# Optimization experiments

Measured on AMD Instinct MI355X. Metric: run time of the kernel, lower is better.

## Reference

```python
import jax, jax.numpy as jnp
import numpy as np

# single species, e3tb basis 1s+1p+1d
FLIST = [1, 3, 5]           # flistnorbs (spin_factor = 1 pre-doubling)
NORB = 9                    # full_basis_norb
SPIN = 2                    # spin_deg -> block doubled
A, E, K = 192, 3072, 4
P = 58                      # sum_{i<=j} iorb*jorb = 1+3+5+9+15+25


def setup_inputs() -> dict:
    key = jax.random.key(0)
    ks = jax.random.split(key, 6)
    return dict(
        orbpair_hopping=jax.random.normal(ks[0], (E, P), jnp.float32),
        orbpair_onsite=jax.random.normal(ks[1], (A, P), jnp.float32),
        R_matrix=jax.random.normal(ks[2], (A, SPIN * NORB, SPIN * NORB), jnp.float32) * 0.1,
        kpoints=jax.random.uniform(ks[3], (K, 3), jnp.float32),
        edge_cell_shift=jax.random.normal(ks[4], (E, 3), jnp.float32),
        edge_index=jax.random.randint(ks[5], (2, E), 0, A, jnp.int64),
    )


def _assemble(feats):
    """Scatter flat orbpair features into upper-triangular [*, NORB, NORB] blocks."""
    n = feats.shape[0]
    H = jnp.zeros((n, NORB, NORB), feats.dtype)
    offs = np.concatenate([[0], np.cumsum(FLIST)])
    p = 0
    for i in range(len(FLIST)):
        for j in range(i, len(FLIST)):
            io, jo = FLIST[i], FLIST[j]
            f = 0.5 if i == j else 1.0  # diagonal orbpairs get 0.5 (hermitianized later)
            H = H.at[:, offs[i]:offs[i] + io, offs[j]:offs[j] + jo].set(
                f * feats[:, p:p + io * jo].reshape(n, io, jo))
            p += io * jo
    return H


def _spin_double(H):
    # H[:, :, 0, :, 0] = H[:, :, 1, :, 1] = H  (kron with eye(2), interleaved layout)
    n = H.shape[0]
    return jnp.einsum('aij,st->aisjt', H, jnp.eye(2, dtype=H.dtype)).reshape(n, SPIN * NORB, SPIN * NORB)


def reference(orbpair_hopping, orbpair_onsite, R_matrix, kpoints, edge_cell_shift, edge_index):
    s = SPIN * NORB
    src, dst = edge_index[0], edge_index[1]

    onsite = _spin_double(_assemble(orbpair_onsite))      # [A, s, s]
    hop = _spin_double(_assemble(orbpair_hopping))        # [E, s, s]

    # rotate: R @ H @ R^T (gathered per-edge for hoppings)
    onsite = jnp.einsum('aip,apq,ajq->aij', R_matrix, onsite, R_matrix)
    hop = jnp.einsum('eip,epq,ejq->eij', R_matrix[src], hop, R_matrix[dst])

    # Bloch phases exp(-2*pi*i k.S) per (k, edge)
    phase = jnp.exp(-2j * jnp.pi * (kpoints @ edge_cell_shift.T)).astype(jnp.complex64)  # [K, E]

    contrib = hop[None].astype(jnp.complex64) * phase[:, :, None, None]  # [K, E, s, s]
    pair = src * A + dst
    blk = jax.vmap(lambda c: jax.ops.segment_sum(c, pair, num_segments=A * A))(contrib)
    blk = blk.reshape(K, A, A, s, s)

    idx = jnp.arange(A)
    blk = blk.at[:, idx, idx].add(onsite[None].astype(jnp.complex64))  # onsite on diag, all k

    Hk = blk.transpose(0, 1, 3, 2, 4).reshape(K, A * s, A * s)
    return Hk + jnp.conj(jnp.swapaxes(Hk, 1, 2))
```

## Files before the change

kernel.cpp:

```cpp
#include <hip/hip_runtime.h>

#define PFEAT 58
#define S18   18
#define ENT   324
#define MAXE  128

__device__ __constant__ unsigned char c_row[PFEAT] = {
    0,0,0,0,0,0,0,0,0,
    1,1,1,2,2,2,3,3,3,
    1,1,1,1,1,2,2,2,2,2,3,3,3,3,3,
    4,4,4,4,4,5,5,5,5,5,6,6,6,6,6,7,7,7,7,7,8,8,8,8,8};
__device__ __constant__ unsigned char c_col[PFEAT] = {
    0,1,2,3,4,5,6,7,8,
    1,2,3,1,2,3,1,2,3,
    4,5,6,7,8,4,5,6,7,8,4,5,6,7,8,
    4,5,6,7,8,4,5,6,7,8,4,5,6,7,8,4,5,6,7,8,4,5,6,7,8};
__device__ __constant__ float c_fac[PFEAT] = {
    0.5f,1,1,1,1,1,1,1,1,
    0.5f,0.5f,0.5f,0.5f,0.5f,0.5f,0.5f,0.5f,0.5f,
    1,1,1,1,1,1,1,1,1,1,1,1,1,1,1,
    0.5f,0.5f,0.5f,0.5f,0.5f,0.5f,0.5f,0.5f,0.5f,0.5f,0.5f,0.5f,0.5f,
    0.5f,0.5f,0.5f,0.5f,0.5f,0.5f,0.5f,0.5f,0.5f,0.5f,0.5f,0.5f};

__device__ __forceinline__ bool detect_i64(const int* __restrict__ ei) {
    const uint2* p = (const uint2*)ei;
    unsigned acc = 0u;
#pragma unroll 8
    for (int m = 0; m < 64; ++m) acc |= p[m].y;
    return acc == 0u;
}

__device__ __forceinline__ int load_idx(const int* __restrict__ ei, int pos,
                                        bool is64, int A) {
    int v = is64 ? ei[2 * pos] : ei[pos];
    v = v < 0 ? 0 : (v >= A ? A - 1 : v);
    return v;
}

__device__ __forceinline__ void assemble_rotate(
    const float* __restrict__ feat, const float* __restrict__ Rs,
    const float* __restrict__ Rd, float* sH9, float* sRs, float* sRd,
    float* sT, float* sM, int t, int nthreads)
{
    for (int idx = t; idx < ENT; idx += nthreads) { sRs[idx] = Rs[idx]; sRd[idx] = Rd[idx]; }
    if (t < 81) sH9[t] = 0.f;
    __syncthreads();
    if (t < PFEAT) sH9[c_row[t] * 9 + c_col[t]] = c_fac[t] * feat[t];
    __syncthreads();

    for (int idx = t; idx < ENT; idx += nthreads) {
        const int pp = idx / S18, q = idx - pp * S18;
        const int i = pp >> 1, u = pp & 1;
        float acc = 0.f;
#pragma unroll
        for (int j = 0; j < 9; ++j)
            acc += sH9[i * 9 + j] * sRd[q * S18 + 2 * j + u];
        sT[idx] = acc;
    }
    __syncthreads();

    for (int idx = t; idx < ENT; idx += nthreads) {
        const int p = idx / S18, q = idx - p * S18;
        float acc = 0.f;
#pragma unroll
        for (int pp = 0; pp < S18; ++pp)
            acc += sRs[p * S18 + pp] * sT[pp * S18 + q];
        sM[idx] = acc;
    }
}


__global__ __launch_bounds__(256) void build_csr_kernel(
    const int* __restrict__ ei, int E, int A,
    int* __restrict__ offsets,
    int2* __restrict__ entries)
{
    extern __shared__ int smem[];
    int* scnt = smem;
    int* scur = smem + A;
    __shared__ int sflag;
    const int t = threadIdx.x;
    if (t == 0) sflag = detect_i64(ei) ? 1 : 0;
    for (int a = t; a < A; a += 256) scnt[a] = 0;
    __syncthreads();
    const bool s64 = sflag != 0;
    for (int e = t; e < E; e += 256) {
        const int a = load_idx(ei, e, s64, A);
        const int b = load_idx(ei, E + e, s64, A);
        atomicAdd(&scnt[a], 1);
        atomicAdd(&scnt[b], 1);
    }
    __syncthreads();
    if (t == 0) {
        int acc = 0;
        for (int a = 0; a < A; ++a) { scur[a] = acc; acc += scnt[a]; }
    }
    __syncthreads();
    for (int a = t; a < A; a += 256) offsets[a] = scur[a];
    if (t == 0) offsets[A] = scur[A - 1] + scnt[A - 1];
    __syncthreads();
    for (int e = t; e < E; e += 256) {
        const int a = load_idx(ei, e, s64, A);
        const int b = load_idx(ei, E + e, s64, A);
        const int p = atomicAdd(&scur[a], 1);
        entries[p] = make_int2(e, b);
        const int q = atomicAdd(&scur[b], 1);
        entries[q] = make_int2(e | (1 << 30), a);
    }
}

__global__ __launch_bounds__(128) void rotate_kernel(
    const float* __restrict__ hop_feat, const float* __restrict__ ons_feat,
    const float* __restrict__ R, const int* __restrict__ ei,
    const float* __restrict__ kpts, const float* __restrict__ shift,
    float* __restrict__ hop_rot, float* __restrict__ hop_rotT,
    float* __restrict__ ons_rot, float* __restrict__ pcos,
    float* __restrict__ psin, int E, int A, int K, int hasT)
{
    __shared__ float sH9[81];
    __shared__ float sRs[ENT];
    __shared__ float sRd[ENT];
    __shared__ float sT[ENT];
    __shared__ float sM[ENT];
    __shared__ int   sflag;

    const int item = blockIdx.x;
    const int t = threadIdx.x;
    if (t == 0) sflag = detect_i64(ei) ? 1 : 0;
    __syncthreads();
    const bool s64 = sflag != 0;

    const float* feat; const float* Rs; const float* Rd; float* outp;
    if (item < E) {
        const int a_s = load_idx(ei, item, s64, A);
        const int a_d = load_idx(ei, E + item, s64, A);
        feat = hop_feat + (size_t)item * PFEAT;
        Rs = R + (size_t)a_s * ENT;
        Rd = R + (size_t)a_d * ENT;
        outp = hop_rot + (size_t)item * ENT;
        for (int k = t; k < K; k += 128) {
            const float dot = kpts[k * 3 + 0] * shift[3 * item + 0]
                            + kpts[k * 3 + 1] * shift[3 * item + 1]
                            + kpts[k * 3 + 2] * shift[3 * item + 2];
            float sv, cv;
            sincosf(-6.28318530717958647692f * dot, &sv, &cv);
            pcos[item * K + k] = cv;
            psin[item * K + k] = sv;
        }
    } else {
        const int a = item - E;
        feat = ons_feat + (size_t)a * PFEAT;
        Rs = R + (size_t)a * ENT;
        Rd = Rs;
        outp = ons_rot + (size_t)a * ENT;
    }

    assemble_rotate(feat, Rs, Rd, sH9, sRs, sRd, sT, sM, t, 128);
    __syncthreads();

    for (int idx = t; idx < ENT; idx += 128) outp[idx] = sM[idx];
    if (item < E && hasT) {
        float* outpT = hop_rotT + (size_t)item * ENT;
        for (int idx = t; idx < ENT; idx += 128) {
            const int p = idx / S18, q = idx - p * S18;
            outpT[idx] = sM[q * S18 + p];
        }
    }
}

__global__ __launch_bounds__(256) void write_kernel(
    const float* __restrict__ hop_rot,
    const float* __restrict__ hop_rotT,
    const float* __restrict__ ons_rot,
    const int*   __restrict__ offsets,
    const int2*  __restrict__ entries,
    const float* __restrict__ pcos,
    const float* __restrict__ psin,
    float* __restrict__ outf,
    int A, int K, int cplx, int hasT, long long lim)
{
    extern __shared__ float rowbuf[];
    __shared__ int2  sent[MAXE];
    __shared__ float sphc[MAXE];
    __shared__ float sphs[MAXE];
    __shared__ float sons[ENT];

    const int N = A * S18;
    const int a    = blockIdx.x >> 1;
    const int half = blockIdx.x & 1;
    const int k = blockIdx.y;
    const int t = threadIdx.x;
    const int i0 = half * 9;
    const int stride = cplx ? 2 : 1;
    const int nbuf = stride * N;
    const int nbuf4 = nbuf >> 2;

    const int beg = offsets[a], end = offsets[a + 1];
    const int cnt = end - beg;
    const int nst = cnt < MAXE ? cnt : MAXE;
    for (int n = t; n < nst; n += 256) {
        const int2 ent = entries[beg + n];
        sent[n] = ent;
        const int e0 = ent.x & 0x3FFFFFFF;
        sphc[n] = pcos[e0 * K + k];
        if (cplx) sphs[n] = psin[e0 * K + k];
    }
    for (int idx = t; idx < ENT; idx += 256) sons[idx] = ons_rot[a * ENT + idx];
    __syncthreads();

    float4* rb4 = (float4*)rowbuf;
    const int total = cnt * S18;

    for (int ri = 0; ri < 9; ++ri) {
        const int i = i0 + ri;
        for (int idx = t; idx < nbuf4; idx += 256)
            rb4[idx] = make_float4(0.f, 0.f, 0.f, 0.f);
        __syncthreads();

        if (t < S18)
            atomicAdd(&rowbuf[stride * (a * S18 + t)],
                      sons[i * S18 + t] + sons[t * S18 + i]);

        for (int m = t; m < total; m += 256) {
            const int n = m / S18, l = m - n * S18;
            int2 ent; float pc, ps = 0.f;
            if (n < MAXE) {
                ent = sent[n]; pc = sphc[n]; if (cplx) ps = sphs[n];
            } else {
                ent = entries[beg + n];
                const int e0 = ent.x & 0x3FFFFFFF;
                pc = pcos[e0 * K + k]; if (cplx) ps = psin[e0 * K + k];
            }
            const int conjf = (ent.x >> 30) & 1;
            const int e = ent.x & 0x3FFFFFFF;
            const int b = ent.y;
            float v;
            if (!conjf)     v = hop_rot [(size_t)e * ENT + i * S18 + l];
            else if (hasT)  v = hop_rotT[(size_t)e * ENT + i * S18 + l];
            else            v = hop_rot [(size_t)e * ENT + l * S18 + i];
            atomicAdd(&rowbuf[stride * (b * S18 + l)], v * pc);
            if (cplx)
                atomicAdd(&rowbuf[stride * (b * S18 + l) + 1], conjf ? -v * ps : v * ps);
        }
        __syncthreads();

        const long long base = (long long)stride
                             * ((long long)k * N + (long long)a * S18 + i)
                             * (long long)N;
        float* dst = outf + base;
        if (base + nbuf <= lim && ((base & 3) == 0)) {
            float4* d4 = (float4*)dst;
            for (int idx = t; idx < nbuf4; idx += 256) d4[idx] = rb4[idx];
        } else {
            for (int idx = t; idx < nbuf; idx += 256)
                if (base + idx < lim) dst[idx] = rowbuf[idx];
        }
        __syncthreads();
    }
}


__global__ __launch_bounds__(256) void zero_kernel(float* __restrict__ p, long long n)
{
    const long long i4 = ((long long)blockIdx.x * 256 + threadIdx.x) * 4;
    if (i4 + 3 < n) {
        *(float4*)(p + i4) = make_float4(0.f, 0.f, 0.f, 0.f);
    } else if (i4 < n) {
        for (long long i = i4; i < n; ++i) p[i] = 0.f;
    }
}

__global__ __launch_bounds__(256) void edge_kernel(
    const float* __restrict__ hop_feat, const float* __restrict__ R,
    const float* __restrict__ kpts, const float* __restrict__ shift,
    const int* __restrict__ edge_index, float* __restrict__ outf,
    int E, int A, int K, int cplx, long long lim)
{
    __shared__ float sH9[81];
    __shared__ float sRs[ENT];
    __shared__ float sRd[ENT];
    __shared__ float sT[ENT];
    __shared__ float sM[ENT];
    __shared__ float sC[8];
    __shared__ float sS[8];

    const int e = blockIdx.x;
    const int t = threadIdx.x;
    const int N = A * S18;
    const long long N2 = (long long)N * N;

    const bool is64 = detect_i64(edge_index);
    const int a = load_idx(edge_index, e, is64, A);
    const int b = load_idx(edge_index, E + e, is64, A);

    if (t < K && t < 8) {
        const float sx = shift[e * 3 + 0], sy = shift[e * 3 + 1], sz = shift[e * 3 + 2];
        const float dot = kpts[t * 3 + 0] * sx + kpts[t * 3 + 1] * sy + kpts[t * 3 + 2] * sz;
        float sv, cv;
        sincosf(-6.28318530717958647692f * dot, &sv, &cv);
        sC[t] = cv; sS[t] = sv;
    }

    assemble_rotate(hop_feat + (size_t)e * PFEAT,
                    R + (size_t)a * ENT, R + (size_t)b * ENT,
                    sH9, sRs, sRd, sT, sM, t, 256);
    __syncthreads();

    const int total = K * ENT;
    for (int idx = t; idx < total; idx += 256) {
        const int k = idx / ENT, r = idx - k * ENT;
        const int i = r / S18, j = r - i * S18;
        const float v = sM[r];
        const float re = v * sC[k];
        const float im = v * sS[k];
        const long long I = (long long)a * S18 + i;
        const long long J = (long long)b * S18 + j;
        const long long p1 = k * N2 + I * N + J;
        const long long p2 = k * N2 + J * N + I;
        if (cplx) {
            if (2 * p1 + 1 < lim) { atomicAdd(&outf[2 * p1], re); atomicAdd(&outf[2 * p1 + 1], im); }
            if (2 * p2 + 1 < lim) { atomicAdd(&outf[2 * p2], re); atomicAdd(&outf[2 * p2 + 1], -im); }
        } else {
            if (p1 < lim) atomicAdd(&outf[p1], re);
            if (p2 < lim) atomicAdd(&outf[p2], re);
        }
    }
}

__global__ __launch_bounds__(128) void onsite_kernel(
    const float* __restrict__ ons_feat, const float* __restrict__ R,
    float* __restrict__ outf, int A, int K, int cplx, long long lim)
{
    __shared__ float sH9[81];
    __shared__ float sRs[ENT];
    __shared__ float sRd[ENT];
    __shared__ float sT[ENT];
    __shared__ float sM[ENT];

    const int a = blockIdx.x;
    const int t = threadIdx.x;
    const int N = A * S18;
    const long long N2 = (long long)N * N;

    assemble_rotate(ons_feat + (size_t)a * PFEAT,
                    R + (size_t)a * ENT, R + (size_t)a * ENT,
                    sH9, sRs, sRd, sT, sM, t, 128);
    __syncthreads();

    for (int idx = t; idx < ENT; idx += 128) {
        const int i = idx / S18, j = idx - (idx / S18) * S18;
        const float v = sM[i * S18 + j] + sM[j * S18 + i];
        const long long I = (long long)a * S18 + i;
        const long long J = (long long)a * S18 + j;
        for (int k = 0; k < K; ++k) {
            const long long p1 = k * N2 + I * N + J;
            const long long off = cplx ? 2 * p1 : p1;
            if (off < lim) outf[off] += v;
        }
    }
}

extern "C" void kernel_launch(void* const* d_in, const int* in_sizes, int n_in,
                              void* d_out, int out_size, void* d_ws, size_t ws_size,
                              hipStream_t stream) {
    const float* hop_feat   = (const float*)d_in[0];
    const float* ons_feat   = (const float*)d_in[1];
    const float* R          = (const float*)d_in[2];
    const float* kpts       = (const float*)d_in[3];
    const float* shift      = (const float*)d_in[4];
    const int*   edge_index = (const int*)d_in[5];

    const int E = in_sizes[0] / PFEAT;
    const int A = in_sizes[1] / PFEAT;
    const int K = in_sizes[3] / 3;

    const long long N  = (long long)A * S18;
    const long long n_real = (long long)K * N * N;
    const long long lim = (long long)out_size;
    const int cplx = (lim >= 2 * n_real) ? 1 : 0;

    float* outf = (float*)d_out;

    char* ws = (char*)d_ws;
    const size_t off_hop = 0;
    const size_t off_ons = off_hop + (size_t)E * ENT * 4;
    const size_t off_ent = off_ons + (size_t)A * ENT * 4;
    const size_t off_off = off_ent + (size_t)2 * E * 8;
    const size_t off_pc  = off_off + (size_t)(A + 2) * 4;
    const size_t off_ps  = off_pc  + (size_t)E * K * 4;
    const size_t base_need = off_ps + (size_t)E * K * 4;
    const size_t off_hT  = base_need;
    const size_t full_need = off_hT + (size_t)E * ENT * 4;

    if (ws_size >= base_need && A <= 4096 && (A & 1) == 0) {
        const int hasT = (ws_size >= full_need) ? 1 : 0;
        float* hop_rot  = (float*)(ws + off_hop);
        float* ons_rot  = (float*)(ws + off_ons);
        int2*  entries  = (int2*)(ws + off_ent);
        int*   offsets  = (int*)(ws + off_off);
        float* pcos     = (float*)(ws + off_pc);
        float* psin     = (float*)(ws + off_ps);
        float* hop_rotT = (float*)(ws + off_hT);

        build_csr_kernel<<<1, 256, 2 * A * sizeof(int), stream>>>(edge_index, E, A,
                                                                  offsets, entries);
        rotate_kernel<<<E + A, 128, 0, stream>>>(hop_feat, ons_feat, R, edge_index,
                                                 kpts, shift, hop_rot, hop_rotT,
                                                 ons_rot, pcos, psin, E, A, K, hasT);
        const size_t shmem = (size_t)(cplx ? 2 : 1) * N * sizeof(float);
        dim3 grid((unsigned)(A * 2), (unsigned)K);
        write_kernel<<<grid, 256, shmem, stream>>>(hop_rot, hop_rotT, ons_rot,
                                                   offsets, entries, pcos, psin,
                                                   outf, A, K, cplx, hasT, lim);
    } else {
        const long long n4 = (lim + 3) / 4;
        const int zgrid = (int)((n4 + 255) / 256);
        zero_kernel<<<zgrid, 256, 0, stream>>>(outf, lim);
        edge_kernel<<<E, 256, 0, stream>>>(hop_feat, R, kpts, shift, edge_index,
                                           outf, E, A, K, cplx, lim);
        onsite_kernel<<<A, 128, 0, stream>>>(ons_feat, R, outf, A, K, cplx, lim);
    }
}
```

Baseline: 262.6 us.

## Fuse k-points into write kernel with column-half split and parallel CSR scan

Measured after the change: 266.4 us. About the same (+1.5%).

```diff
diff --git a/kernel.cpp b/kernel.cpp
--- a/kernel.cpp
+++ b/kernel.cpp
@@ -76,8 +76,9 @@
     int2* __restrict__ entries)
 {
     extern __shared__ int smem[];
-    int* scnt = smem;
-    int* scur = smem + A;
+    int* scnt  = smem;
+    int* scur  = smem + A;
+    int* sscan = smem + 2 * A;
     __shared__ int sflag;
     const int t = threadIdx.x;
     if (t == 0) sflag = detect_i64(ei) ? 1 : 0;
@@ -91,13 +92,27 @@
         atomicAdd(&scnt[b], 1);
     }
     __syncthreads();
-    if (t == 0) {
-        int acc = 0;
-        for (int a = 0; a < A; ++a) { scur[a] = acc; acc += scnt[a]; }
+    if (A <= 256) {
+        const int x = (t < A) ? scnt[t] : 0;
+        sscan[t] = x;
+        __syncthreads();
+        for (int off = 1; off < 256; off <<= 1) {
+            const int y = (t >= off) ? sscan[t - off] : 0;
+            __syncthreads();
+            sscan[t] += y;
+            __syncthreads();
+        }
+        if (t < A) scur[t] = sscan[t] - x;
+        if (t == 255) offsets[A] = sscan[255];
+    } else {
+        if (t == 0) {
+            int acc = 0;
+            for (int a = 0; a < A; ++a) { scur[a] = acc; acc += scnt[a]; }
+            offsets[A] = acc;
+        }
     }
     __syncthreads();
     for (int a = t; a < A; a += 256) offsets[a] = scur[a];
-    if (t == 0) offsets[A] = scur[A - 1] + scnt[A - 1];
     __syncthreads();
     for (int e = t; e < E; e += 256) {
         const int a = load_idx(ei, e, s64, A);
@@ -168,15 +183,106 @@
     }
 }
 
-__global__ __launch_bounds__(256) void write_kernel(
+__global__ __launch_bounds__(512) void write_fused_kernel(
     const float* __restrict__ hop_rot,
     const float* __restrict__ hop_rotT,
     const float* __restrict__ ons_rot,
     const int*   __restrict__ offsets,
     const int2*  __restrict__ entries,
     const float* __restrict__ pcos,
-    const float* __restrict__ psin,
     float* __restrict__ outf,
+    int A, int K, int hasT, long long lim)
+{
+    extern __shared__ float rowbuf[];
+    __shared__ int2  sent[MAXE];
+    __shared__ float sphc[MAXE * 4];
+    __shared__ float sons[ENT];
+
+    const int N = A * S18;
+    const int a    = blockIdx.x >> 1;
+    const int half = blockIdx.x & 1;
+    const int colhalf = blockIdx.y;
+    const int ncolat = A >> 1;
+    const int ncols = ncolat * S18;
+    const int colbase18 = colhalf * ncols;
+    const int t = threadIdx.x;
+    const int i0 = half * 9;
+
+    const int beg = offsets[a];
+    const int cnt = offsets[a + 1] - beg;
+    const int nst = cnt < MAXE ? cnt : MAXE;
+    for (int n = t; n < nst; n += 512) {
+        const int2 ent = entries[beg + n];
+        sent[n] = ent;
+        const int e0 = ent.x & 0x3FFFFFFF;
+        for (int k = 0; k < K; ++k) sphc[n * 4 + k] = pcos[e0 * K + k];
+    }
+    for (int idx = t; idx < ENT; idx += 512) sons[idx] = ons_rot[a * ENT + idx];
+    __syncthreads();
+
+    float4* rb4 = (float4*)rowbuf;
+    const int nz4 = (K * ncols) >> 2;
+    const int total = cnt * S18;
+    const int adiag0 = a * S18 - colbase18;
+    const bool adiag = (adiag0 >= 0) && (adiag0 < ncols);
+
+    for (int ri = 0; ri < 9; ++ri) {
+        const int i = i0 + ri;
+        for (int idx = t; idx < nz4; idx += 512)
+            rb4[idx] = make_float4(0.f, 0.f, 0.f, 0.f);
+        __syncthreads();
+
+        if (adiag && t < S18) {
+            const float v = sons[i * S18 + t] + sons[t * S18 + i];
+            const int c0 = adiag0 + t;
+            for (int k = 0; k < K; ++k) atomicAdd(&rowbuf[k * ncols + c0], v);
+        }
+
+        for (int m = t; m < total; m += 512) {
+            const int n = m / S18, l = m - n * S18;
+            int2 ent;
+            if (n < MAXE) ent = sent[n]; else ent = entries[beg + n];
+            const int c0 = ent.y * S18 - colbase18 + l;
+            if ((unsigned)c0 >= (unsigned)ncols) continue;
+            const int conjf = (ent.x >> 30) & 1;
+            const int e = ent.x & 0x3FFFFFFF;
+            float v;
+            if (!conjf)     v = hop_rot [(size_t)e * ENT + i * S18 + l];
+            else if (hasT)  v = hop_rotT[(size_t)e * ENT + i * S18 + l];
+            else            v = hop_rot [(size_t)e * ENT + l * S18 + i];
+            if (n < MAXE) {
+                for (int k = 0; k < K; ++k)
+                    atomicAdd(&rowbuf[k * ncols + c0], v * sphc[n * 4 + k]);
+            } else {
+                for (int k = 0; k < K; ++k)
+                    atomicAdd(&rowbuf[k * ncols + c0], v * pcos[e * K + k]);
+            }
+        }
+        __syncthreads();
+
+        const long long I = (long long)a * S18 + i;
+        for (int k = 0; k < K; ++k) {
+            const long long base = ((long long)k * N + I) * N + colbase18;
+            float* dst = outf + base;
+            const float* src = rowbuf + k * ncols;
+            if (base + ncols <= lim) {
+                float4* d4 = (float4*)dst;
+                const float4* s4 = (const float4*)src;
+                for (int idx = t; idx < (ncols >> 2); idx += 512) d4[idx] = s4[idx];
+            } else {
+                for (int idx = t; idx < ncols; idx += 512)
+                    if (base + idx < lim) dst[idx] = src[idx];
+            }
+        }
+        __syncthreads();
+    }
+}
+
+__global__ __launch_bounds__(256) void write_kernel(
+    const float* __restrict__ hop_rot, const float* __restrict__ hop_rotT,
+    const float* __restrict__ ons_rot, const int* __restrict__ offsets,
+    const int2* __restrict__ entries, const float* __restrict__ pcos,
+    const float* __restrict__ psin, float* __restrict__ outf,
     int A, int K, int cplx, int hasT, long long lim)
 {
     extern __shared__ float rowbuf[];
@@ -402,16 +508,28 @@
         float* psin     = (float*)(ws + off_ps);
         float* hop_rotT = (float*)(ws + off_hT);
 
-        build_csr_kernel<<<1, 256, 2 * A * sizeof(int), stream>>>(edge_index, E, A,
-                                                                  offsets, entries);
+        const size_t csr_smem = (size_t)(2 * A + 256) * sizeof(int);
+        build_csr_kernel<<<1, 256, csr_smem, stream>>>(edge_index, E, A,
+                                                       offsets, entries);
         rotate_kernel<<<E + A, 128, 0, stream>>>(hop_feat, ons_feat, R, edge_index,
                                                  kpts, shift, hop_rot, hop_rotT,
                                                  ons_rot, pcos, psin, E, A, K, hasT);
-        const size_t shmem = (size_t)(cplx ? 2 : 1) * N * sizeof(float);
-        dim3 grid((unsigned)(A * 2), (unsigned)K);
-        write_kernel<<<grid, 256, shmem, stream>>>(hop_rot, hop_rotT, ons_rot,
-                                                   offsets, entries, pcos, psin,
-                                                   outf, A, K, cplx, hasT, lim);
+
+        const size_t fused_smem = (size_t)K * (A / 2) * S18 * sizeof(float);
+        const bool fastw = (cplx == 0) && (K >= 1) && (K <= 4) && ((A & 3) == 0)
+                           && (fused_smem <= 60 * 1024);
+        if (fastw) {
+            dim3 grid((unsigned)(A * 2), 2u);
+            write_fused_kernel<<<grid, 512, fused_smem, stream>>>(
+                hop_rot, hop_rotT, ons_rot, offsets, entries, pcos,
+                outf, A, K, hasT, lim);
+        } else {
+            const size_t shmem = (size_t)(cplx ? 2 : 1) * N * sizeof(float);
+            dim3 grid((unsigned)(A * 2), (unsigned)K);
+            write_kernel<<<grid, 256, shmem, stream>>>(hop_rot, hop_rotT, ons_rot,
+                                                       offsets, entries, pcos, psin,
+                                                       outf, A, K, cplx, hasT, lim);
+        }
     } else {
         const long long n4 = (lim + 3) / 4;
         const int zgrid = (int)((n4 + 255) / 256);
```

## Fold CSR build into prep kernel and add column-parallel real-output writer

Applied to the files above, without the earlier changes.

Result: faster. 226.9 us (-13.6%).

```diff
diff --git a/kernel.cpp b/kernel.cpp
--- a/kernel.cpp
+++ b/kernel.cpp
@@ -4,6 +4,7 @@
 #define S18   18
 #define ENT   324
 #define MAXE  128
+#define MAXA  256
 
 __device__ __constant__ unsigned char c_row[PFEAT] = {
     0,0,0,0,0,0,0,0,0,
@@ -70,58 +71,22 @@
 }
 
 
-__global__ __launch_bounds__(256) void build_csr_kernel(
-    const int* __restrict__ ei, int E, int A,
-    int* __restrict__ offsets,
-    int2* __restrict__ entries)
-{
-    extern __shared__ int smem[];
-    int* scnt = smem;
-    int* scur = smem + A;
-    __shared__ int sflag;
-    const int t = threadIdx.x;
-    if (t == 0) sflag = detect_i64(ei) ? 1 : 0;
-    for (int a = t; a < A; a += 256) scnt[a] = 0;
-    __syncthreads();
-    const bool s64 = sflag != 0;
-    for (int e = t; e < E; e += 256) {
-        const int a = load_idx(ei, e, s64, A);
-        const int b = load_idx(ei, E + e, s64, A);
-        atomicAdd(&scnt[a], 1);
-        atomicAdd(&scnt[b], 1);
-    }
-    __syncthreads();
-    if (t == 0) {
-        int acc = 0;
-        for (int a = 0; a < A; ++a) { scur[a] = acc; acc += scnt[a]; }
-    }
-    __syncthreads();
-    for (int a = t; a < A; a += 256) offsets[a] = scur[a];
-    if (t == 0) offsets[A] = scur[A - 1] + scnt[A - 1];
-    __syncthreads();
-    for (int e = t; e < E; e += 256) {
-        const int a = load_idx(ei, e, s64, A);
-        const int b = load_idx(ei, E + e, s64, A);
-        const int p = atomicAdd(&scur[a], 1);
-        entries[p] = make_int2(e, b);
-        const int q = atomicAdd(&scur[b], 1);
-        entries[q] = make_int2(e | (1 << 30), a);
-    }
-}
-
-__global__ __launch_bounds__(128) void rotate_kernel(
+__global__ __launch_bounds__(128) void prep_kernel(
     const float* __restrict__ hop_feat, const float* __restrict__ ons_feat,
     const float* __restrict__ R, const int* __restrict__ ei,
     const float* __restrict__ kpts, const float* __restrict__ shift,
     float* __restrict__ hop_rot, float* __restrict__ hop_rotT,
     float* __restrict__ ons_rot, float* __restrict__ pcos,
-    float* __restrict__ psin, int E, int A, int K, int hasT)
+    float* __restrict__ psin, int* __restrict__ offsets,
+    int2* __restrict__ entries, int E, int A, int K, int hasT)
 {
     __shared__ float sH9[81];
     __shared__ float sRs[ENT];
     __shared__ float sRd[ENT];
     __shared__ float sT[ENT];
     __shared__ float sM[ENT];
+    __shared__ int   scnt[MAXA];
+    __shared__ int   scur[MAXA];
     __shared__ int   sflag;
 
     const int item = blockIdx.x;
@@ -129,6 +94,33 @@
     if (t == 0) sflag = detect_i64(ei) ? 1 : 0;
     __syncthreads();
     const bool s64 = sflag != 0;
+
+    if (item == E + A) {
+        for (int a = t; a < A; a += 128) scnt[a] = 0;
+        __syncthreads();
+        for (int e = t; e < E; e += 128) {
+            const int a = load_idx(ei, e, s64, A);
+            const int b = load_idx(ei, E + e, s64, A);
+            atomicAdd(&scnt[a], 1);
+            atomicAdd(&scnt[b], 1);
+        }
+        __syncthreads();
+        if (t == 0) {
+            int acc = 0;
+            for (int a = 0; a < A; ++a) { scur[a] = acc; offsets[a] = acc; acc += scnt[a]; }
+            offsets[A] = acc;
+        }
+        __syncthreads();
+        for (int e = t; e < E; e += 128) {
+            const int a = load_idx(ei, e, s64, A);
+            const int b = load_idx(ei, E + e, s64, A);
+            const int p = atomicAdd(&scur[a], 1);
+            entries[p] = make_int2(e, b);
+            const int q = atomicAdd(&scur[b], 1);
+            entries[q] = make_int2(e | (1 << 30), a);
+        }
+        return;
+    }
 
     const float* feat; const float* Rs; const float* Rd; float* outp;
     if (item < E) {
@@ -168,15 +160,88 @@
     }
 }
 
-__global__ __launch_bounds__(256) void write_kernel(
+__global__ __launch_bounds__(384) void writer_cols_kernel(
     const float* __restrict__ hop_rot,
     const float* __restrict__ hop_rotT,
     const float* __restrict__ ons_rot,
     const int*   __restrict__ offsets,
     const int2*  __restrict__ entries,
     const float* __restrict__ pcos,
-    const float* __restrict__ psin,
     float* __restrict__ outf,
+    int A, int K, long long lim)
+{
+    __shared__ int   se[MAXE];
+    __shared__ int   sb[MAXE];
+    __shared__ float spc[MAXE];
+    __shared__ float sons[ENT];
+
+    const int N = A * S18;
+    const int a = blockIdx.z;
+    const int k = blockIdx.y;
+    const int t = threadIdx.x;
+    const int c = blockIdx.x * 384 + t;
+
+    const int beg = offsets[a];
+    const int cnt = offsets[a + 1] - beg;
+    const int nst = cnt < MAXE ? cnt : MAXE;
+    for (int n = t; n < nst; n += 384) {
+        const int2 ent = entries[beg + n];
+        se[n] = ent.x;
+        sb[n] = ent.y;
+        spc[n] = pcos[(ent.x & 0x3FFFFFFF) * K + k];
+    }
+    for (int idx = t; idx < ENT; idx += 384) sons[idx] = ons_rot[a * ENT + idx];
+    __syncthreads();
+
+    if (c >= N) return;
+    const int b = c / S18, l = c - b * S18;
+
+    float acc[S18];
+    if (b == a) {
+#pragma unroll
+        for (int i = 0; i < S18; ++i)
+            acc[i] = sons[i * S18 + l] + sons[l * S18 + i];
+    } else {
+#pragma unroll
+        for (int i = 0; i < S18; ++i) acc[i] = 0.f;
+    }
+
+    for (int n = 0; n < nst; ++n) {
+        if (sb[n] != b) continue;
+        const int ex = se[n];
+        const int e = ex & 0x3FFFFFFF;
+        const float pc = spc[n];
+        const float* base = ((ex >> 30) & 1)
+                          ? (hop_rot  + (size_t)e * ENT + l * S18)
+                          : (hop_rotT + (size_t)e * ENT + l * S18);
+#pragma unroll
+        for (int i = 0; i < S18; ++i) acc[i] += base[i] * pc;
+    }
+    for (int n = MAXE; n < cnt; ++n) {
+        const int2 ent = entries[beg + n];
+        if (ent.y != b) continue;
+        const int e = ent.x & 0x3FFFFFFF;
+        const float pc = pcos[e * K + k];
+        const float* base = ((ent.x >> 30) & 1)
+                          ? (hop_rot  + (size_t)e * ENT + l * S18)
+                          : (hop_rotT + (size_t)e * ENT + l * S18);
+#pragma unroll
+        for (int i = 0; i < S18; ++i) acc[i] += base[i] * pc;
+    }
+
+    const long long rowbase = ((long long)k * N + (long long)a * S18) * (long long)N + c;
+#pragma unroll
+    for (int i = 0; i < S18; ++i) {
+        const long long off = rowbase + (long long)i * N;
+        if (off < lim) outf[off] = acc[i];
+    }
+}
+
+__global__ __launch_bounds__(256) void write_kernel(
+    const float* __restrict__ hop_rot, const float* __restrict__ hop_rotT,
+    const float* __restrict__ ons_rot, const int* __restrict__ offsets,
+    const int2* __restrict__ entries, const float* __restrict__ pcos,
+    const float* __restrict__ psin, float* __restrict__ outf,
     int A, int K, int cplx, int hasT, long long lim)
 {
     extern __shared__ float rowbuf[];
@@ -392,7 +457,7 @@
     const size_t off_hT  = base_need;
     const size_t full_need = off_hT + (size_t)E * ENT * 4;
 
-    if (ws_size >= base_need && A <= 4096 && (A & 1) == 0) {
+    if (ws_size >= base_need && A <= MAXA) {
         const int hasT = (ws_size >= full_need) ? 1 : 0;
         float* hop_rot  = (float*)(ws + off_hop);
         float* ons_rot  = (float*)(ws + off_ons);
@@ -402,16 +467,24 @@
         float* psin     = (float*)(ws + off_ps);
         float* hop_rotT = (float*)(ws + off_hT);
 
-        build_csr_kernel<<<1, 256, 2 * A * sizeof(int), stream>>>(edge_index, E, A,
-                                                                  offsets, entries);
-        rotate_kernel<<<E + A, 128, 0, stream>>>(hop_feat, ons_feat, R, edge_index,
-                                                 kpts, shift, hop_rot, hop_rotT,
-                                                 ons_rot, pcos, psin, E, A, K, hasT);
-        const size_t shmem = (size_t)(cplx ? 2 : 1) * N * sizeof(float);
-        dim3 grid((unsigned)(A * 2), (unsigned)K);
-        write_kernel<<<grid, 256, shmem, stream>>>(hop_rot, hop_rotT, ons_rot,
-                                                   offsets, entries, pcos, psin,
-                                                   outf, A, K, cplx, hasT, lim);
+        prep_kernel<<<E + A + 1, 128, 0, stream>>>(
+            hop_feat, ons_feat, R, edge_index, kpts, shift,
+            hop_rot, hop_rotT, ons_rot, pcos, psin, offsets, entries,
+            E, A, K, hasT);
+
+        if (cplx == 0 && hasT) {
+            const int nchunks = (int)((N + 383) / 384);
+            dim3 grid((unsigned)nchunks, (unsigned)K, (unsigned)A);
+            writer_cols_kernel<<<grid, 384, 0, stream>>>(
+                hop_rot, hop_rotT, ons_rot, offsets, entries, pcos,
+                outf, A, K, lim);
+        } else {
+            const size_t shmem = (size_t)(cplx ? 2 : 1) * N * sizeof(float);
+            dim3 grid((unsigned)(A * 2), (unsigned)K);
+            write_kernel<<<grid, 256, shmem, stream>>>(hop_rot, hop_rotT, ons_rot,
+                                                       offsets, entries, pcos, psin,
+                                                       outf, A, K, cplx, hasT, lim);
+        }
     } else {
         const long long n4 = (lim + 3) / 4;
         const int zgrid = (int)((n4 + 255) / 256);
```
